# Optimization experiments

Hardware: AMD Instinct MI355X
Metric: run time of the kernel (lower is better)

Reference implementation:

```python
import jax, jax.numpy as jnp
import numpy as np

N_HEADS = 16


def setup_inputs() -> dict:
    key = jax.random.key(0)
    ks = jax.random.split(key, 5)
    B, S, D = 2, 2048, 1024
    x = jax.random.normal(ks[0], (B, S, D), dtype=jnp.float32)
    Wqkv = jax.random.normal(ks[1], (D, 3 * D), dtype=jnp.float32) * (1.0 / np.sqrt(D))
    bqkv = jax.random.normal(ks[2], (3 * D,), dtype=jnp.float32) * 0.02
    Wout = jax.random.normal(ks[3], (D, D), dtype=jnp.float32) * (1.0 / np.sqrt(D))
    bout = jax.random.normal(ks[4], (D,), dtype=jnp.float32) * 0.02
    return {"x": x, "Wqkv": Wqkv, "bqkv": bqkv, "Wout": Wout, "bout": bout}


def reference(x, Wqkv, bqkv, Wout, bout):
    B, S, D = x.shape
    H = N_HEADS
    dh = D // H
    # qkv projection, then view as [B,S,H,3*dh] and chunk on last dim
    # (matches torch: per-head q/k/v are interleaved slices of the projection)
    qkv = (x @ Wqkv + bqkv).reshape(B, S, H, 3 * dh).transpose(0, 2, 1, 3)  # [B,H,S,3dh]
    q, k, v = jnp.split(qkv, 3, axis=-1)  # each [B,H,S,dh]
    scale = jnp.asarray(1.0 / np.sqrt(dh), dtype=x.dtype)
    scores = jnp.einsum('bhqd,bhkd->bhqk', q, k) * scale  # [B,H,S,S]
    causal = jnp.tril(jnp.ones((S, S), dtype=bool))
    scores = jnp.where(causal, scores, jnp.asarray(-jnp.inf, dtype=scores.dtype))
    attn_w = jax.nn.softmax(scores, axis=-1)
    attn = jnp.einsum('bhqk,bhkd->bhqd', attn_w, v)  # [B,H,S,dh]
    attn = attn.transpose(0, 2, 1, 3).reshape(B, S, D)
    return attn @ Wout + bout
```

## Files before the change

### kernel.cpp

```cpp
#include <hip/hip_runtime.h>
#include <hip/hip_bf16.h>
#include <cstdint>
#include <cstddef>

typedef __hip_bfloat16 bf16;
typedef short bf16x4 __attribute__((ext_vector_type(4)));
typedef short bf16x8 __attribute__((ext_vector_type(8)));
typedef float f32x4 __attribute__((ext_vector_type(4)));

#define LOG2E 1.44269504088896f

static constexpr int Bb = 2, S = 2048, D = 1024, H = 16, DH = 64;

struct TrueT  { static constexpr bool value = true;  };
struct FalseT { static constexpr bool value = false; };

__device__ inline short f2bf_bits(float f) {
  bf16 b = __float2bfloat16(f);
  short s;
  __builtin_memcpy(&s, &b, 2);
  return s;
}
__device__ inline float bfbits2f(short s) {
  uint32_t u = ((uint32_t)(uint16_t)s) << 16;
  float f;
  __builtin_memcpy(&f, &u, 4);
  return f;
}

__global__ __launch_bounds__(256) void prep_kernel(
    const float* __restrict__ Wqkv, bf16* __restrict__ wqkvT,
    const float* __restrict__ Wout, bf16* __restrict__ woutT,
    const float* __restrict__ x, bf16* __restrict__ xbf) {
  const int blk = blockIdx.x;
  const int tid = threadIdx.x;
  if (blk < 4096) {
    __shared__ float t[32][33];
    const float* in;
    bf16* out;
    int R, C, bx, by;
    if (blk < 3072) { in = Wqkv; out = wqkvT; R = 1024; C = 3072; bx = blk % 96; by = blk / 96; }
    else            { in = Wout; out = woutT; R = 1024; C = 1024; bx = (blk - 3072) % 32; by = (blk - 3072) / 32; }
    int c0 = bx * 32, r0 = by * 32;
    int tx = tid & 31, ty = tid >> 5;
#pragma unroll
    for (int i = 0; i < 4; i++) {
      int r = ty + i * 8;
      t[r][tx] = in[(size_t)(r0 + r) * C + c0 + tx];
    }
    __syncthreads();
#pragma unroll
    for (int i = 0; i < 4; i++) {
      int c = ty + i * 8;
      out[(size_t)(c0 + c) * R + r0 + tx] = __float2bfloat16(t[tx][c]);
    }
  } else {
    size_t i = ((size_t)(blk - 4096) * 256 + tid) * 8;
    f32x4 a = *(const f32x4*)(x + i);
    f32x4 b = *(const f32x4*)(x + i + 4);
    bf16x8 v;
#pragma unroll
    for (int j = 0; j < 4; j++) { v[j] = f2bf_bits(a[j]); v[4 + j] = f2bf_bits(b[j]); }
    *(bf16x8*)((short*)xbf + i) = v;
  }
}

__global__ __launch_bounds__(256) void gemm_qkv(
    const bf16* __restrict__ A, const bf16* __restrict__ Bt,
    const float* __restrict__ bias,
    bf16* __restrict__ Qb, bf16* __restrict__ Kb, bf16* __restrict__ Vtb) {
  constexpr int K = 1024;
  __shared__ __align__(16) short smA[128 * 32];
  __shared__ __align__(16) short smB[128 * 32];
  __shared__ __align__(16) short smE[4][16 * 72];

  const int tid = threadIdx.x;
  const int wave = tid >> 6, lane = tid & 63;
  const int quad = lane >> 4, l16 = lane & 15;
  const int m0 = blockIdx.y * 128, n0 = blockIdx.x * 128;
  const int wm = wave >> 1, wn = wave & 1;

  f32x4 acc[4][4];
#pragma unroll
  for (int i = 0; i < 4; i++)
#pragma unroll
    for (int j = 0; j < 4; j++) acc[i][j] = {0.f, 0.f, 0.f, 0.f};

  const int srow = lane >> 2;
  const int scol = ((lane & 3) ^ ((lane >> 3) & 3)) * 8;
  const int gsw = (l16 >> 1) & 3;

  for (int k0 = 0; k0 < K; k0 += 32) {
#pragma unroll
    for (int half = 0; half < 2; half++) {
      int row = half * 64 + wave * 16 + srow;
      const bf16* ga = A + (size_t)(m0 + row) * K + k0 + scol;
      const bf16* gb = Bt + (size_t)(n0 + row) * K + k0 + scol;
      __builtin_amdgcn_global_load_lds(
          (const __attribute__((address_space(1))) void*)ga,
          (__attribute__((address_space(3))) void*)&smA[(half * 64 + wave * 16) * 32],
          16, 0, 0);
      __builtin_amdgcn_global_load_lds(
          (const __attribute__((address_space(1))) void*)gb,
          (__attribute__((address_space(3))) void*)&smB[(half * 64 + wave * 16) * 32],
          16, 0, 0);
    }
    __syncthreads();

    bf16x8 af[4], bf_[4];
#pragma unroll
    for (int mi = 0; mi < 4; mi++)
      af[mi] = *(const bf16x8*)&smA[(wm * 64 + mi * 16 + l16) * 32 + (quad ^ gsw) * 8];
#pragma unroll
    for (int ni = 0; ni < 4; ni++)
      bf_[ni] = *(const bf16x8*)&smB[(wn * 64 + ni * 16 + l16) * 32 + (quad ^ gsw) * 8];
#pragma unroll
    for (int mi = 0; mi < 4; mi++)
#pragma unroll
      for (int ni = 0; ni < 4; ni++)
        acc[mi][ni] = __builtin_amdgcn_mfma_f32_16x16x32_bf16(
            af[mi], bf_[ni], acc[mi][ni], 0, 0, 0);
    __syncthreads();
  }

  const int cs0 = n0 + wn * 64;
  const int h = cs0 / 192;
  const int rt = (cs0 >> 6) % 3;
  const int t0w = m0 + wm * 64;
  const int b = t0w >> 11, s0w = t0w & 2047;

  float bv[4];
#pragma unroll
  for (int ni = 0; ni < 4; ni++) bv[ni] = bias[cs0 + ni * 16 + l16];

  if (rt < 2) {
    const float qscale = (rt == 0) ? (0.125f * LOG2E) : 1.0f;
    bf16* dst = (rt == 0 ? Qb : Kb) + ((size_t)(b * H + h) * S + s0w) * 64;
    short* sE = &smE[wave][0];
    const int r8 = lane >> 2, s4 = lane & 3;
#pragma unroll
    for (int mi = 0; mi < 4; mi++) {
#pragma unroll
      for (int ni = 0; ni < 4; ni++)
#pragma unroll
        for (int r = 0; r < 4; r++)
          sE[(quad * 4 + r) * 72 + ni * 16 + l16] =
              f2bf_bits((acc[mi][ni][r] + bv[ni]) * qscale);
      asm volatile("s_waitcnt lgkmcnt(0)" ::: "memory");
      bf16x8 w0 = *(const bf16x8*)&sE[r8 * 72 + s4 * 16];
      bf16x8 w1 = *(const bf16x8*)&sE[r8 * 72 + s4 * 16 + 8];
      short* g = (short*)dst + (size_t)(mi * 16 + r8) * 64 + s4 * 16;
      *(bf16x8*)g = w0;
      *(bf16x8*)(g + 8) = w1;
      asm volatile("s_waitcnt lgkmcnt(0)" ::: "memory");
    }
  } else {
#pragma unroll
    for (int ni = 0; ni < 4; ni++) {
      const int dh = ni * 16 + l16;
#pragma unroll
      for (int mi = 0; mi < 4; mi++) {
        const int s0 = s0w + mi * 16 + quad * 4;
        size_t base = ((size_t)(b * H + h) * 64 + dh) * S + s0;
        bf16x4 vv;
#pragma unroll
        for (int r = 0; r < 4; r++) vv[r] = f2bf_bits(acc[mi][ni][r] + bv[ni]);
        *(bf16x4*)((short*)Vtb + base) = vv;
      }
    }
  }
}

__global__ __launch_bounds__(256) void gemm_out(
    const bf16* __restrict__ A, const bf16* __restrict__ Bt,
    const float* __restrict__ bias, float* __restrict__ C,
    int M, int N, int K) {
  constexpr int BN = 64, NF = 2;
  __shared__ __align__(16) short smA[128 * 32];
  __shared__ __align__(16) short smB[BN * 32];
  __shared__ __align__(16) float smEf[4][580];

  const int tid = threadIdx.x;
  const int wave = tid >> 6, lane = tid & 63;
  const int quad = lane >> 4, l16 = lane & 15;
  const int m0 = blockIdx.y * 128, n0 = blockIdx.x * BN;
  const int wm = wave >> 1, wn = wave & 1;

  f32x4 acc[4][NF];
#pragma unroll
  for (int i = 0; i < 4; i++)
#pragma unroll
    for (int j = 0; j < NF; j++) acc[i][j] = {0.f, 0.f, 0.f, 0.f};

  const int srow = lane >> 2;
  const int scol = ((lane & 3) ^ ((lane >> 3) & 3)) * 8;
  const int gsw = (l16 >> 1) & 3;

  for (int k0 = 0; k0 < K; k0 += 32) {
#pragma unroll
    for (int half = 0; half < 2; half++) {
      int row = half * 64 + wave * 16 + srow;
      const bf16* ga = A + (size_t)(m0 + row) * K + k0 + scol;
      __builtin_amdgcn_global_load_lds(
          (const __attribute__((address_space(1))) void*)ga,
          (__attribute__((address_space(3))) void*)&smA[(half * 64 + wave * 16) * 32],
          16, 0, 0);
    }
    {
      int row = wave * 16 + srow;
      const bf16* gb = Bt + (size_t)(n0 + row) * K + k0 + scol;
      __builtin_amdgcn_global_load_lds(
          (const __attribute__((address_space(1))) void*)gb,
          (__attribute__((address_space(3))) void*)&smB[(wave * 16) * 32],
          16, 0, 0);
    }
    __syncthreads();

    bf16x8 af[4], bf_[NF];
#pragma unroll
    for (int mi = 0; mi < 4; mi++)
      af[mi] = *(const bf16x8*)&smA[(wm * 64 + mi * 16 + l16) * 32 + (quad ^ gsw) * 8];
#pragma unroll
    for (int ni = 0; ni < NF; ni++)
      bf_[ni] = *(const bf16x8*)&smB[(wn * 32 + ni * 16 + l16) * 32 + (quad ^ gsw) * 8];
#pragma unroll
    for (int mi = 0; mi < 4; mi++)
#pragma unroll
      for (int ni = 0; ni < NF; ni++)
        acc[mi][ni] = __builtin_amdgcn_mfma_f32_16x16x32_bf16(
            af[mi], bf_[ni], acc[mi][ni], 0, 0, 0);
    __syncthreads();
  }

  float bv[NF];
#pragma unroll
  for (int ni = 0; ni < NF; ni++) bv[ni] = bias[n0 + wn * 32 + ni * 16 + l16];

  float* sE = &smEf[wave][0];
#pragma unroll
  for (int mi = 0; mi < 4; mi++) {
#pragma unroll
    for (int ni = 0; ni < NF; ni++)
#pragma unroll
      for (int r = 0; r < 4; r++)
        sE[(quad * 4 + r) * 36 + ni * 16 + l16] = acc[mi][ni][r] + bv[ni];
    asm volatile("s_waitcnt lgkmcnt(0)" ::: "memory");
#pragma unroll
    for (int t = 0; t < 2; t++) {
      int slot = t * 64 + lane;
      int rr = slot >> 3, c4 = slot & 7;
      f32x4 v = *(const f32x4*)&sE[rr * 36 + c4 * 4];
      int row = m0 + wm * 64 + mi * 16 + rr;
      int col = n0 + wn * 32 + c4 * 4;
      *(f32x4*)&C[(size_t)row * N + col] = v;
    }
    asm volatile("s_waitcnt lgkmcnt(0)" ::: "memory");
  }
}

__global__ __launch_bounds__(256) void attn_kernel(
    const bf16* __restrict__ Qb, const bf16* __restrict__ Kb,
    const bf16* __restrict__ Vtb,
    bf16* __restrict__ Op0, bf16* __restrict__ Op1,
    float* __restrict__ lp0, float* __restrict__ lp1,
    bf16* __restrict__ Ofinal, int split) {
  const int blk = blockIdx.x;
  const int xcd = blk & 7;
  const int idx = blk >> 3;
  int sk, p, bh;
  if (split == 2) { bh = xcd + 8 * (idx / 32); int r = idx % 32; p = r & 15; sk = r >> 4; }
  else            { bh = xcd + 8 * (idx / 16); p = idx & 15; sk = 0; }
  const int h = bh & (H - 1), b = bh >> 4;
  const int tid = threadIdx.x;
  const int wave = tid >> 6, lane = tid & 63;
  const int quad = lane >> 4, l16 = lane & 15;

  bf16*  __restrict__ Op = sk ? Op1 : Op0;
  float* __restrict__ lp = sk ? lp1 : lp0;

  const bf16* Qh = Qb + (size_t)(b * H + h) * S * 64;
  const bf16* Kh = Kb + (size_t)(b * H + h) * S * 64;
  const bf16* Vth = Vtb + (size_t)(b * H + h) * 64 * S;

  __shared__ __align__(16) short smK[2][64 * 64];
  __shared__ __align__(16) short smVt[64 * 64];
  __shared__ __align__(16) short pLds[4][16][76];

  const int lrow = lane >> 3;
  const int lg = lane & 7;
  const int swz = l16 & 7;

  bf16x8 onesB;
#pragma unroll
  for (int j = 0; j < 8; j++) onesB[j] = (short)0x3F80;

  auto stageK = [&](int it2, int bufi) {
    const int kv0 = it2 * 64;
#pragma unroll
    for (int j = 0; j < 2; j++) {
      const int row = wave * 16 + j * 8 + lrow;
      const bf16* ks = Kh + (size_t)(kv0 + row) * 64 + (lg ^ (row & 7)) * 8;
      __builtin_amdgcn_global_load_lds(
          (const __attribute__((address_space(1))) void*)ks,
          (__attribute__((address_space(3))) void*)&smK[bufi][(wave * 16 + j * 8) * 64],
          16, 0, 0);
    }
  };
  auto stageV = [&](int it2) {
    const int kv0 = it2 * 64;
#pragma unroll
    for (int j = 0; j < 2; j++) {
      const int row = wave * 16 + j * 8 + lrow;
      const bf16* vs = Vth + (size_t)row * S + kv0 + (lg ^ (row & 7)) * 8;
      __builtin_amdgcn_global_load_lds(
          (const __attribute__((address_space(1))) void*)vs,
          (__attribute__((address_space(3))) void*)&smVt[(wave * 16 + j * 8) * 64],
          16, 0, 0);
    }
  };

#pragma unroll
  for (int pass = 0; pass < 2; pass++) {
    const int qt = pass ? p : (31 - p);
    const int q0 = qt * 64 + wave * 16;
    const int qglob = q0 + l16;

    bf16x8 aQ[2];
#pragma unroll
    for (int kh = 0; kh < 2; kh++)
      aQ[kh] = *(const bf16x8*)(Qh + (size_t)(q0 + l16) * 64 + kh * 32 + quad * 8);

    f32x4 o[4];
#pragma unroll
    for (int dt = 0; dt < 4; dt++) o[dt] = {0.f, 0.f, 0.f, 0.f};
    f32x4 lacc = {0.f, 0.f, 0.f, 0.f};

    auto qk_softmax = [&](int it2, int bufi, auto diag_tag) {
      constexpr bool DIAG = decltype(diag_tag)::value;
      const int kv0 = it2 * 64;
      f32x4 z[4];
      __builtin_amdgcn_s_setprio(1);
#pragma unroll
      for (int nh = 0; nh < 4; nh++) {
        const int row = nh * 16 + l16;
        f32x4 t = {0.f, 0.f, 0.f, 0.f};
#pragma unroll
        for (int kh = 0; kh < 2; kh++) {
          bf16x8 bK = *(const bf16x8*)&smK[bufi][row * 64 + ((kh * 4 + quad) ^ swz) * 8];
          t = __builtin_amdgcn_mfma_f32_16x16x32_bf16(bK, aQ[kh], t, 0, 0, 0);
        }
        z[nh] = t;
      }
      __builtin_amdgcn_s_setprio(0);

#pragma unroll
      for (int nh = 0; nh < 4; nh++) {
        bf16x4 pk;
#pragma unroll
        for (int r = 0; r < 4; r++) {
          float e = exp2f(z[nh][r]);
          if (DIAG) {
            const int kidx = kv0 + nh * 16 + quad * 4 + r;
            e = (kidx <= qglob) ? e : 0.f;
          }
          pk[r] = f2bf_bits(e);
        }
        *(bf16x4*)&pLds[wave][l16][nh * 16 + quad * 4] = pk;
      }
      asm volatile("s_waitcnt lgkmcnt(0)" ::: "memory");
    };

    auto pv = [&]() {
      bf16x8 aP[2];
#pragma unroll
      for (int k2 = 0; k2 < 2; k2++)
        aP[k2] = *(const bf16x8*)&pLds[wave][l16][k2 * 32 + quad * 8];
      __builtin_amdgcn_s_setprio(1);
#pragma unroll
      for (int k2 = 0; k2 < 2; k2++)
        lacc = __builtin_amdgcn_mfma_f32_16x16x32_bf16(aP[k2], onesB, lacc, 0, 0, 0);
#pragma unroll
      for (int dt = 0; dt < 4; dt++) {
        const int row = dt * 16 + l16;
#pragma unroll
        for (int k2 = 0; k2 < 2; k2++) {
          bf16x8 bV = *(const bf16x8*)&smVt[row * 64 + ((k2 * 4 + quad) ^ swz) * 8];
          o[dt] = __builtin_amdgcn_mfma_f32_16x16x32_bf16(aP[k2], bV, o[dt], 0, 0, 0);
        }
      }
      __builtin_amdgcn_s_setprio(0);
    };

    int it = sk;
    __syncthreads();
    if (it <= qt) stageK(it, 0);
    __syncthreads();
    int cur = 0;
    while (it <= qt) {
      const int next = it + split;
      const bool hn = (next <= qt);
      stageV(it);
      if (hn) stageK(next, cur ^ 1);
      if (it == qt) qk_softmax(it, cur, TrueT{});
      else          qk_softmax(it, cur, FalseT{});
      if (hn) { asm volatile("s_waitcnt vmcnt(2)" ::: "memory"); }
      else    { asm volatile("s_waitcnt vmcnt(0)" ::: "memory"); }
      __builtin_amdgcn_s_barrier();
      asm volatile("" ::: "memory");
      pv();
      __syncthreads();
      cur ^= 1;
      it = next;
    }

    short* pw = &pLds[wave][0][0];
    if (split > 1) {
      const size_t rowbase = (size_t)(b * H + h) * S + q0;
      if (l16 == 0) {
#pragma unroll
        for (int r = 0; r < 4; r++) lp[rowbase + quad * 4 + r] = lacc[r];
      }
#pragma unroll
      for (int dt = 0; dt < 4; dt++)
#pragma unroll
        for (int r = 0; r < 4; r++)
          pw[(quad * 4 + r) * 76 + dt * 16 + l16] = f2bf_bits(o[dt][r]);
      asm volatile("s_waitcnt lgkmcnt(0)" ::: "memory");
      {
        const int rl = lane >> 2, cq = lane & 3;
        bf16x8 w0 = *(const bf16x8*)&pw[rl * 76 + cq * 16];
        bf16x8 w1 = *(const bf16x8*)&pw[rl * 76 + cq * 16 + 8];
        short* g = (short*)Op + (rowbase + rl) * 64 + cq * 16;
        *(bf16x8*)g = w0;
        *(bf16x8*)(g + 8) = w1;
      }
      asm volatile("s_waitcnt lgkmcnt(0)" ::: "memory");
    } else {
      float inv[4];
#pragma unroll
      for (int r = 0; r < 4; r++) inv[r] = 1.f / lacc[r];
#pragma unroll
      for (int dt = 0; dt < 4; dt++)
#pragma unroll
        for (int r = 0; r < 4; r++)
          pw[(quad * 4 + r) * 76 + dt * 16 + l16] = f2bf_bits(o[dt][r] * inv[r]);
      asm volatile("s_waitcnt lgkmcnt(0)" ::: "memory");
      {
        const int rl = lane >> 2, cq = lane & 3;
        bf16x8 w0 = *(const bf16x8*)&pw[rl * 76 + cq * 16];
        bf16x8 w1 = *(const bf16x8*)&pw[rl * 76 + cq * 16 + 8];
        short* g = (short*)Ofinal + (size_t)(b * S + q0 + rl) * D + h * 64 + cq * 16;
        *(bf16x8*)g = w0;
        *(bf16x8*)(g + 8) = w1;
      }
      asm volatile("s_waitcnt lgkmcnt(0)" ::: "memory");
    }
  }
}

__global__ __launch_bounds__(256) void attn_reduce(
    const bf16* __restrict__ O0, const bf16* __restrict__ O1,
    const float* __restrict__ l0, const float* __restrict__ l1,
    bf16* __restrict__ attnO) {
  int gid = blockIdx.x * 256 + threadIdx.x;
  int row = gid >> 3;
  int c8 = (gid & 7) * 8;
  float inv = 1.f / (l0[row] + l1[row]);
  bf16x8 a = *(const bf16x8*)((const short*)O0 + (size_t)row * 64 + c8);
  bf16x8 bb = *(const bf16x8*)((const short*)O1 + (size_t)row * 64 + c8);
  bf16x8 o;
#pragma unroll
  for (int j = 0; j < 8; j++)
    o[j] = f2bf_bits((bfbits2f(a[j]) + bfbits2f(bb[j])) * inv);
  int bh = row >> 11, q = row & 2047;
  int b = bh >> 4, h = bh & 15;
  *(bf16x8*)((short*)attnO + (((size_t)(b * S + q) * H + h) * 64 + c8)) = o;
}

extern "C" void kernel_launch(void* const* d_in, const int* in_sizes, int n_in,
                              void* d_out, int out_size, void* d_ws, size_t ws_size,
                              hipStream_t stream) {
  const float* x    = (const float*)d_in[0];
  const float* Wqkv = (const float*)d_in[1];
  const float* bqkv = (const float*)d_in[2];
  const float* Wout = (const float*)d_in[3];
  const float* bout = (const float*)d_in[4];
  float* out = (float*)d_out;

  char* ws = (char*)d_ws;
  const bool split2 = (ws_size >= 50855936);

  bf16* Qb  = (bf16*)(ws);
  bf16* Kb  = (bf16*)(ws + 8388608);
  bf16* Vtb = (bf16*)(ws + 16777216);
  bf16* xbf = (bf16*)(ws + 25165824);

  bf16 *Op0 = nullptr, *Op1 = nullptr, *attnO;
  float *lp0 = nullptr, *lp1 = nullptr;
  bf16 *wqkvT, *woutT;
  if (split2) {
    Op0   = (bf16*)(ws + 25165824);
    Op1   = (bf16*)(ws + 33554432);
    lp0   = (float*)(ws + 41943040);
    lp1   = (float*)(ws + 42205184);
    attnO = (bf16*)(ws + 8388608);
    wqkvT = (bf16*)(ws + 42467328);
    woutT = (bf16*)(ws + 48758784);
  } else {
    attnO = (bf16*)(ws + 25165824);
    wqkvT = (bf16*)(ws + 33554432);
    woutT = (bf16*)(ws + 39845888);
  }

  prep_kernel<<<dim3(6144), 256, 0, stream>>>(Wqkv, wqkvT, Wout, woutT, x, xbf);

  gemm_qkv<<<dim3(3072 / 128, 4096 / 128), 256, 0, stream>>>(
      xbf, wqkvT, bqkv, Qb, Kb, Vtb);

  if (split2) {
    attn_kernel<<<dim3(1024), 256, 0, stream>>>(
        Qb, Kb, Vtb, Op0, Op1, lp0, lp1, nullptr, 2);
    attn_reduce<<<dim3(2048), 256, 0, stream>>>(Op0, Op1, lp0, lp1, attnO);
  } else {
    attn_kernel<<<dim3(512), 256, 0, stream>>>(
        Qb, Kb, Vtb, nullptr, nullptr, nullptr, nullptr, attnO, 1);
  }

  gemm_out<<<dim3(1024 / 64, 4096 / 128), 256, 0, stream>>>(
      attnO, woutT, bout, out, 4096, 1024, 1024);
}
```

Before: 183.9 us.

## Double-buffer LDS tiles in QKV and output projection GEMMs

Both projection GEMMs now keep two LDS buffers for the A and B tiles. The global-to-LDS loads for the next k-slice are issued before the MFMA work on the current slice, so copy latency can overlap with compute instead of stalling on a barrier before every slice. This doubles the LDS staging footprint per block, which may lower occupancy. It relies on the end-of-iteration barrier waiting for the outstanding async LDS loads.

```diff
diff --git a/kernel.cpp b/kernel.cpp
--- a/kernel.cpp
+++ b/kernel.cpp
@@ -70,8 +70,8 @@
     const float* __restrict__ bias,
     bf16* __restrict__ Qb, bf16* __restrict__ Kb, bf16* __restrict__ Vtb) {
   constexpr int K = 1024;
-  __shared__ __align__(16) short smA[128 * 32];
-  __shared__ __align__(16) short smB[128 * 32];
+  __shared__ __align__(16) short smA[2][128 * 32];
+  __shared__ __align__(16) short smB[2][128 * 32];
   __shared__ __align__(16) short smE[4][16 * 72];
 
   const int tid = threadIdx.x;
@@ -90,7 +90,7 @@
   const int scol = ((lane & 3) ^ ((lane >> 3) & 3)) * 8;
   const int gsw = (l16 >> 1) & 3;
 
-  for (int k0 = 0; k0 < K; k0 += 32) {
+  auto stage = [&](int k0, int bufi) {
 #pragma unroll
     for (int half = 0; half < 2; half++) {
       int row = half * 64 + wave * 16 + srow;
@@ -98,22 +98,28 @@
       const bf16* gb = Bt + (size_t)(n0 + row) * K + k0 + scol;
       __builtin_amdgcn_global_load_lds(
           (const __attribute__((address_space(1))) void*)ga,
-          (__attribute__((address_space(3))) void*)&smA[(half * 64 + wave * 16) * 32],
+          (__attribute__((address_space(3))) void*)&smA[bufi][(half * 64 + wave * 16) * 32],
           16, 0, 0);
       __builtin_amdgcn_global_load_lds(
           (const __attribute__((address_space(1))) void*)gb,
-          (__attribute__((address_space(3))) void*)&smB[(half * 64 + wave * 16) * 32],
+          (__attribute__((address_space(3))) void*)&smB[bufi][(half * 64 + wave * 16) * 32],
           16, 0, 0);
     }
-    __syncthreads();
+  };
+
+  stage(0, 0);
+  __syncthreads();
+  int cur = 0;
+  for (int k0 = 0; k0 < K; k0 += 32) {
+    if (k0 + 32 < K) stage(k0 + 32, cur ^ 1);
 
     bf16x8 af[4], bf_[4];
 #pragma unroll
     for (int mi = 0; mi < 4; mi++)
-      af[mi] = *(const bf16x8*)&smA[(wm * 64 + mi * 16 + l16) * 32 + (quad ^ gsw) * 8];
+      af[mi] = *(const bf16x8*)&smA[cur][(wm * 64 + mi * 16 + l16) * 32 + (quad ^ gsw) * 8];
 #pragma unroll
     for (int ni = 0; ni < 4; ni++)
-      bf_[ni] = *(const bf16x8*)&smB[(wn * 64 + ni * 16 + l16) * 32 + (quad ^ gsw) * 8];
+      bf_[ni] = *(const bf16x8*)&smB[cur][(wn * 64 + ni * 16 + l16) * 32 + (quad ^ gsw) * 8];
 #pragma unroll
     for (int mi = 0; mi < 4; mi++)
 #pragma unroll
@@ -121,6 +127,7 @@
         acc[mi][ni] = __builtin_amdgcn_mfma_f32_16x16x32_bf16(
             af[mi], bf_[ni], acc[mi][ni], 0, 0, 0);
     __syncthreads();
+    cur ^= 1;
   }
 
   const int cs0 = n0 + wn * 64;
@@ -176,8 +183,8 @@
     const float* __restrict__ bias, float* __restrict__ C,
     int M, int N, int K) {
   constexpr int BN = 64, NF = 2;
-  __shared__ __align__(16) short smA[128 * 32];
-  __shared__ __align__(16) short smB[BN * 32];
+  __shared__ __align__(16) short smA[2][128 * 32];
+  __shared__ __align__(16) short smB[2][BN * 32];
   __shared__ __align__(16) float smEf[4][580];
 
   const int tid = threadIdx.x;
@@ -196,14 +203,14 @@
   const int scol = ((lane & 3) ^ ((lane >> 3) & 3)) * 8;
   const int gsw = (l16 >> 1) & 3;
 
-  for (int k0 = 0; k0 < K; k0 += 32) {
+  auto stage = [&](int k0, int bufi) {
 #pragma unroll
     for (int half = 0; half < 2; half++) {
       int row = half * 64 + wave * 16 + srow;
       const bf16* ga = A + (size_t)(m0 + row) * K + k0 + scol;
       __builtin_amdgcn_global_load_lds(
           (const __attribute__((address_space(1))) void*)ga,
-          (__attribute__((address_space(3))) void*)&smA[(half * 64 + wave * 16) * 32],
+          (__attribute__((address_space(3))) void*)&smA[bufi][(half * 64 + wave * 16) * 32],
           16, 0, 0);
     }
     {
@@ -211,18 +218,24 @@
       const bf16* gb = Bt + (size_t)(n0 + row) * K + k0 + scol;
       __builtin_amdgcn_global_load_lds(
           (const __attribute__((address_space(1))) void*)gb,
-          (__attribute__((address_space(3))) void*)&smB[(wave * 16) * 32],
+          (__attribute__((address_space(3))) void*)&smB[bufi][(wave * 16) * 32],
           16, 0, 0);
     }
-    __syncthreads();
+  };
+
+  stage(0, 0);
+  __syncthreads();
+  int cur = 0;
+  for (int k0 = 0; k0 < K; k0 += 32) {
+    if (k0 + 32 < K) stage(k0 + 32, cur ^ 1);
 
     bf16x8 af[4], bf_[NF];
 #pragma unroll
     for (int mi = 0; mi < 4; mi++)
-      af[mi] = *(const bf16x8*)&smA[(wm * 64 + mi * 16 + l16) * 32 + (quad ^ gsw) * 8];
+      af[mi] = *(const bf16x8*)&smA[cur][(wm * 64 + mi * 16 + l16) * 32 + (quad ^ gsw) * 8];
 #pragma unroll
     for (int ni = 0; ni < NF; ni++)
-      bf_[ni] = *(const bf16x8*)&smB[(wn * 32 + ni * 16 + l16) * 32 + (quad ^ gsw) * 8];
+      bf_[ni] = *(const bf16x8*)&smB[cur][(wn * 32 + ni * 16 + l16) * 32 + (quad ^ gsw) * 8];
 #pragma unroll
     for (int mi = 0; mi < 4; mi++)
 #pragma unroll
@@ -230,6 +243,7 @@
         acc[mi][ni] = __builtin_amdgcn_mfma_f32_16x16x32_bf16(
             af[mi], bf_[ni], acc[mi][ni], 0, 0, 0);
     __syncthreads();
+    cur ^= 1;
   }
 
   float bv[NF];
```

After: 181.8 us. Within noise of the previous version (-1.1%).
